# Kernel tuning notes

Hardware: AMD Instinct MI355X
Metric: run time of the kernel (lower is better)

The kernel has to match this reference:

```python
import jax, jax.numpy as jnp
import numpy as np

B, H, NI, NQ = 4096, 1024, 4096, 2048


def setup_inputs() -> dict:
    key = jax.random.key(0)
    ks = jax.random.split(key, 12)
    state = jax.random.normal(ks[0], (B, H), jnp.float32)
    inputX = jax.random.normal(ks[1], (B, NI), jnp.float32)
    # one-hot next-question vector
    q_idx = jax.random.randint(ks[2], (B,), 0, NQ)
    inputY = jax.nn.one_hot(q_idx, NQ, dtype=jnp.float32)
    truth = jax.random.bernoulli(ks[3], 0.5, (B,)).astype(jnp.float32)
    # torch.nn.Linear default init: U(-1/sqrt(fan_in), 1/sqrt(fan_in)), weight (out,in)
    def lin(kw, kb, out_d, in_d):
        bound = 1.0 / np.sqrt(in_d)
        W = jax.random.uniform(kw, (out_d, in_d), jnp.float32, -bound, bound)
        b = jax.random.uniform(kb, (out_d,), jnp.float32, -bound, bound)
        return W, b
    W_t, b_t = lin(ks[4], ks[5], H, H)    # transfer: n_hidden -> n_hidden
    W_x, b_x = lin(ks[6], ks[7], H, NI)   # linear_x: n_input -> n_hidden
    W_y, b_y = lin(ks[8], ks[9], NQ, H)   # linear_y: n_hidden -> n_questions
    return {"state": state, "inputX": inputX, "inputY": inputY, "truth": truth,
            "W_t": W_t, "b_t": b_t, "W_x": W_x, "b_x": b_x, "W_y": W_y, "b_y": b_y}


def reference(state, inputX, inputY, truth, W_t, b_t, W_x, b_x, W_y, b_y):
    # two small linears + tanh -> new hidden state
    linM = state @ W_t.T + b_t                       # (B, H)
    linX = inputX @ W_x.T + b_x                      # (B, H)
    hidden = jnp.tanh(linM + linX)                   # (B, H)
    # prediction head: linear + sigmoid, mask-select via one-hot sum
    pred_output = jax.nn.sigmoid(hidden @ W_y.T + b_y)  # (B, NQ)
    pred = jnp.sum(pred_output * inputY, axis=1)        # (B,)
    # binary cross entropy, sum reduction; torch clamps log terms at -100
    log_p = jnp.maximum(jnp.log(pred), -100.0)
    log_1mp = jnp.maximum(jnp.log1p(-pred), -100.0)
    err = -jnp.sum(truth * log_p + (1.0 - truth) * log_1mp)
    return (pred, err, hidden)
```

## Files before the change

kernel.cpp:

```cpp
#include <hip/hip_runtime.h>
#include <stdint.h>
#include <math.h>

#define B_DIM 4096
#define H_DIM 1024
#define NI_DIM 4096
#define NQ_DIM 2048
#define K_DIM 5120
#define NKT 160

typedef __attribute__((ext_vector_type(8))) short short8;
typedef __attribute__((ext_vector_type(4))) float f32x4;

__device__ __forceinline__ unsigned short f2bf(float f) {
  unsigned u = __float_as_uint(f);
  u += 0x7FFFu + ((u >> 16) & 1u);
  return (unsigned short)(u >> 16);
}
__device__ __forceinline__ float bf2f(unsigned short s) {
  return __uint_as_float(((unsigned)s) << 16);
}
__device__ __forceinline__ unsigned pkbf(float a, float b) {
  unsigned r;
  asm("v_cvt_pk_bf16_f32 %0, %1, %2" : "=v"(r) : "v"(a), "v"(b));
  return r;
}

__device__ __forceinline__ void gload_lds16(const void* g, void* l) {
  __builtin_amdgcn_global_load_lds(
      (__attribute__((address_space(1))) void*)(uintptr_t)g,
      (__attribute__((address_space(3))) void*)l, 16, 0, 0);
}

__global__ __launch_bounds__(256) void cast_v4(
    const float* __restrict__ X0, const float* __restrict__ X1,
    const float* __restrict__ W0, const float* __restrict__ W1,
    short* __restrict__ Xc, short* __restrict__ Wc) {
  __shared__ __align__(16) short lds[16384];
  int bt = blockIdx.x;
  const float *s0, *s1;
  short* dst;
  if (bt < (B_DIM / 128) * (NKT / 4)) { s0 = X0; s1 = X1; dst = Xc; }
  else { bt -= (B_DIM / 128) * (NKT / 4); s0 = W0; s1 = W1; dst = Wc; }
  const int rowTile = bt / (NKT / 4);
  const int K0 = (bt % (NKT / 4)) * 4;
  const float* src;
  int cols, colBase;
  if (K0 < 32) { src = s0; cols = 1024; colBase = K0 * 32; }
  else         { src = s1; cols = 4096; colBase = (K0 - 32) * 32; }
  const int tid = threadIdx.x;
  const int kc = tid & 31;
  const int r0 = tid >> 5;
#pragma unroll
  for (int i = 0; i < 16; ++i) {
    int r = r0 + i * 8;
    float4 v = *(const float4*)(src +
        (long long)(rowTile * 128 + r) * cols + colBase + kc * 4);
    uint2 o;
    o.x = pkbf(v.x, v.y);
    o.y = pkbf(v.z, v.w);
    int l = (kc >> 1) * 128 + r;
    int p = l ^ ((l >> 7) & 7);
    *(uint2*)(&lds[p * 8 + (kc & 1) * 4]) = o;
  }
  __syncthreads();
  short* dbase = dst + ((long long)rowTile * NKT + K0) * 4096;
#pragma unroll
  for (int i = 0; i < 8; ++i) {
    int c = tid + i * 256;
    int p = c ^ ((c >> 7) & 7);
    *(short8*)(dbase + c * 8) = *(const short8*)(&lds[p * 8]);
  }
}

__device__ __forceinline__ int ep_swz(int col, int rw) {
  int byte = col * 512 + rw * 2;
  byte ^= ((col ^ (col >> 3)) & 7) << 4;
  return byte;
}

__global__ __launch_bounds__(512, 2) void gemm_256(
    const short* __restrict__ Xc, const short* __restrict__ Wc,
    short* __restrict__ P, int ntile) {
  __shared__ __align__(16) short SH[65536];
  const int tid = threadIdx.x;
  const int lane = tid & 63;
  const int wid = tid >> 6;
  const int wr = wid >> 2, wc = wid & 3;
  const int fr = lane & 15, fq = lane >> 4;

  const int nwg = gridDim.x;
  const int orig = blockIdx.x;
  const int cpx = nwg >> 3;
  const int swz = (orig & 7) * cpx + (orig >> 3);
  const int bz = swz >> 6;
  const int bm = (swz >> 2) & 15;
  const int bn = swz & 3;
  const int kt0 = bz * (2 * ntile);

  const short* gA0 = Xc + ((long long)((bm * 2 + 0) * NKT + kt0) << 12);
  const short* gA2 = Xc + ((long long)((bm * 2 + 1) * NKT + kt0) << 12);
  const short* gB0 = Wc + ((long long)((bn * 2 + 0) * NKT + kt0) << 12);
  const short* gB2 = Wc + ((long long)((bn * 2 + 1) * NKT + kt0) << 12);

  f32x4 acc[8][4] = {};

  const int t8 = tid * 8;

  {
    gload_lds16(gA0 + t8, &SH[t8]);
    gload_lds16(gA0 + 4096 + t8, &SH[4096 + t8]);
    gload_lds16(gA2 + t8, &SH[8192 + t8]);
    gload_lds16(gA2 + 4096 + t8, &SH[12288 + t8]);
    gload_lds16(gB0 + t8, &SH[16384 + t8]);
    gload_lds16(gB0 + 4096 + t8, &SH[20480 + t8]);
    gload_lds16(gB2 + t8, &SH[24576 + t8]);
    gload_lds16(gB2 + 4096 + t8, &SH[28672 + t8]);
  }
  __syncthreads();

  int cur = 0;
  for (int t = 0; t < ntile; ++t) {
    if (t + 1 < ntile) {
      long long off = (long long)(t + 1) * 8192 + t8;
      short* L = &SH[(cur ^ 1) * 32768];
      gload_lds16(gA0 + off, L + t8);
      gload_lds16(gA0 + 4096 + off, L + 4096 + t8);
      gload_lds16(gA2 + off, L + 8192 + t8);
      gload_lds16(gA2 + 4096 + off, L + 12288 + t8);
      gload_lds16(gB0 + off, L + 16384 + t8);
      gload_lds16(gB0 + 4096 + off, L + 20480 + t8);
      gload_lds16(gB2 + off, L + 24576 + t8);
      gload_lds16(gB2 + 4096 + off, L + 28672 + t8);
    }
    const short* aS = &SH[cur * 32768] + wr * 8192;
    const short* bS = &SH[cur * 32768 + 16384] + (wc >> 1) * 8192;
    const int brow = (wc & 1) * 64;
#pragma unroll
    for (int ks = 0; ks < 2; ++ks) {
      short8 av[8], bv[4];
#pragma unroll
      for (int mi = 0; mi < 8; ++mi)
        av[mi] = *(const short8*)(aS + ks * 4096 +
                                  (fq * 128 + mi * 16 + fr) * 8);
#pragma unroll
      for (int ni = 0; ni < 4; ++ni)
        bv[ni] = *(const short8*)(bS + ks * 4096 +
                                  (fq * 128 + brow + ni * 16 + fr) * 8);
#pragma unroll
      for (int mi = 0; mi < 8; ++mi)
#pragma unroll
        for (int ni = 0; ni < 4; ++ni)
          acc[mi][ni] = __builtin_amdgcn_mfma_f32_16x16x32_bf16(
              av[mi], bv[ni], acc[mi][ni], 0, 0, 0);
    }
    __syncthreads();
    cur ^= 1;
  }

#pragma unroll
  for (int ni = 0; ni < 4; ++ni) {
    int col = wc * 64 + ni * 16 + fr;
#pragma unroll
    for (int mi = 0; mi < 8; ++mi) {
      int rw = wr * 128 + mi * 16 + fq * 4;
      uint2 pk;
      pk.x = (unsigned)f2bf(acc[mi][ni][0]) |
             ((unsigned)f2bf(acc[mi][ni][1]) << 16);
      pk.y = (unsigned)f2bf(acc[mi][ni][2]) |
             ((unsigned)f2bf(acc[mi][ni][3]) << 16);
      *(uint2*)((char*)SH + ep_swz(col, rw)) = pk;
    }
  }
  __syncthreads();
  short* Pp = P + (long long)bz * B_DIM * H_DIM;
#pragma unroll
  for (int h = 0; h < 16; ++h) {
    int chunk = tid + h * 512;
    int rr = chunk >> 5;
    int j = chunk & 31;
    short8 o;
#pragma unroll
    for (int k = 0; k < 8; ++k) {
      o[k] = *(const short*)((char*)SH + ep_swz(j * 8 + k, rr));
    }
    *(short8*)(Pp + (long long)(bm * 256 + rr) * H_DIM + bn * 256 + j * 8) = o;
  }
}

__global__ __launch_bounds__(256) void fuse_row(
    const short* __restrict__ P, const float* __restrict__ bt,
    const float* __restrict__ bx, const float* __restrict__ Y,
    const float* __restrict__ truth, const float* __restrict__ Wy,
    const float* __restrict__ by, float* __restrict__ predOut,
    float* __restrict__ hidden, float* __restrict__ bce, int S) {
  const int b = blockIdx.x;
  const int tid = threadIdx.x;
  __shared__ int s_cnt;
  __shared__ int s_idx[8];
  __shared__ float s_val[8];
  __shared__ float s_red[4];
  if (tid == 0) s_cnt = 0;

  const int c = tid * 4;
  float s0 = 0.f, s1 = 0.f, s2 = 0.f, s3 = 0.f;
  for (int z = 0; z < S; ++z) {
    const short* Pr = P + ((long long)z * B_DIM + b) * H_DIM + c;
    uint2 u = *(const uint2*)Pr;
    s0 += bf2f((unsigned short)(u.x & 0xffff));
    s1 += bf2f((unsigned short)(u.x >> 16));
    s2 += bf2f((unsigned short)(u.y & 0xffff));
    s3 += bf2f((unsigned short)(u.y >> 16));
  }
  float4 bt4 = *(const float4*)(bt + c);
  float4 bx4 = *(const float4*)(bx + c);
  float h0 = tanhf(s0 + bt4.x + bx4.x);
  float h1 = tanhf(s1 + bt4.y + bx4.y);
  float h2 = tanhf(s2 + bt4.z + bx4.z);
  float h3 = tanhf(s3 + bt4.w + bx4.w);
  float* Hr = hidden + (long long)b * H_DIM + c;
  Hr[0] = h0; Hr[1] = h1; Hr[2] = h2; Hr[3] = h3;

  __syncthreads();
  const float4* Yr = (const float4*)(Y + (long long)b * NQ_DIM);
#pragma unroll
  for (int hh = 0; hh < NQ_DIM / 4 / 256; ++hh) {
    int j = tid + hh * 256;
    float4 v = Yr[j];
    if (v.x != 0.0f) { int p = atomicAdd(&s_cnt, 1); if (p < 8) { s_idx[p] = 4 * j;     s_val[p] = v.x; } }
    if (v.y != 0.0f) { int p = atomicAdd(&s_cnt, 1); if (p < 8) { s_idx[p] = 4 * j + 1; s_val[p] = v.y; } }
    if (v.z != 0.0f) { int p = atomicAdd(&s_cnt, 1); if (p < 8) { s_idx[p] = 4 * j + 2; s_val[p] = v.z; } }
    if (v.w != 0.0f) { int p = atomicAdd(&s_cnt, 1); if (p < 8) { s_idx[p] = 4 * j + 3; s_val[p] = v.w; } }
  }
  __syncthreads();
  int cnt = s_cnt < 8 ? s_cnt : 8;
  float predv = 0.0f;
  for (int it = 0; it < cnt; ++it) {
    int q = s_idx[it];
    float4 w = *(const float4*)(Wy + (long long)q * H_DIM + c);
    float part = h0 * w.x + h1 * w.y + h2 * w.z + h3 * w.w;
#pragma unroll
    for (int off = 32; off > 0; off >>= 1) part += __shfl_down(part, off, 64);
    if ((tid & 63) == 0) s_red[tid >> 6] = part;
    __syncthreads();
    if (tid == 0) {
      float z = s_red[0] + s_red[1] + s_red[2] + s_red[3] + by[q];
      float p = 1.0f / (1.0f + expf(-z));
      predv += s_val[it] * p;
    }
    __syncthreads();
  }
  if (tid == 0) {
    predOut[b] = predv;
    float t = truth[b];
    float lp = fmaxf(logf(predv), -100.0f);
    float l1p = fmaxf(log1pf(-predv), -100.0f);
    bce[b] = -(t * lp + (1.0f - t) * l1p);
  }
}

__global__ __launch_bounds__(256) void reduce_err(
    const float* __restrict__ bce, float* __restrict__ errOut) {
  float s = 0.0f;
  for (int i = threadIdx.x; i < B_DIM; i += 256) s += bce[i];
#pragma unroll
  for (int off = 32; off > 0; off >>= 1) s += __shfl_down(s, off, 64);
  __shared__ float red[4];
  if ((threadIdx.x & 63) == 0) red[threadIdx.x >> 6] = s;
  __syncthreads();
  if (threadIdx.x == 0) errOut[0] = red[0] + red[1] + red[2] + red[3];
}

extern "C" void kernel_launch(void* const* d_in, const int* in_sizes, int n_in,
                              void* d_out, int out_size, void* d_ws, size_t ws_size,
                              hipStream_t stream) {
  (void)in_sizes; (void)n_in; (void)out_size;
  const float* state  = (const float*)d_in[0];
  const float* inputX = (const float*)d_in[1];
  const float* inputY = (const float*)d_in[2];
  const float* truth  = (const float*)d_in[3];
  const float* W_t    = (const float*)d_in[4];
  const float* b_t    = (const float*)d_in[5];
  const float* W_x    = (const float*)d_in[6];
  const float* b_x    = (const float*)d_in[7];
  const float* W_y    = (const float*)d_in[8];
  const float* b_y    = (const float*)d_in[9];

  const size_t XC_B = (size_t)B_DIM * K_DIM * 2;
  const size_t WC_B = (size_t)H_DIM * K_DIM * 2;
  const size_t PART = (size_t)B_DIM * H_DIM * 2;

  int S = 1;
  if (ws_size >= XC_B + WC_B + 4 * PART + 16384) S = 4;
  else if (ws_size >= XC_B + WC_B + 2 * PART + 16384) S = 2;

  short* Xc = (short*)d_ws;
  short* Wc = (short*)((char*)d_ws + XC_B);
  short* P  = (short*)((char*)d_ws + XC_B + WC_B);
  float* bce = (float*)((char*)d_ws + XC_B + WC_B + (size_t)S * PART);

  float* predOut = (float*)d_out;
  float* errOut  = predOut + B_DIM;
  float* hidden  = predOut + B_DIM + 1;

  cast_v4<<<(B_DIM / 128 + H_DIM / 128) * (NKT / 4), 256, 0, stream>>>(
      state, inputX, W_t, W_x, Xc, Wc);

  gemm_256<<<64 * S, 512, 0, stream>>>(Xc, Wc, P, 80 / S);

  fuse_row<<<B_DIM, 256, 0, stream>>>(P, b_t, b_x, inputY, truth, W_y, b_y,
                                      predOut, hidden, bce, S);
  reduce_err<<<1, 256, 0, stream>>>(bce, errOut);
}
```

Before: 92.51 us.

## Replace double-buffered GEMM loop with 4-slot async load pipeline

The bf16 GEMM main loop moves from a two-buffer scheme with 64-wide K steps to a four-slot ring of 32-wide K tiles, prefetching three tiles ahead. It uses explicit vmcnt waits and raw s_barrier in place of __syncthreads, and raises wave priority around the MFMA block with s_setprio. The goal is to hide global-to-LDS load latency better and keep MFMA issue dense. In exchange it runs twice as many iterations and barriers per K range, and correctness depends on the hand-counted vmcnt values matching the four loads issued per stage.

```diff
diff --git a/kernel.cpp b/kernel.cpp
--- a/kernel.cpp
+++ b/kernel.cpp
@@ -79,9 +79,9 @@
   return byte;
 }
 
-__global__ __launch_bounds__(512, 2) void gemm_256(
+__global__ __launch_bounds__(512, 2) void gemm_256p(
     const short* __restrict__ Xc, const short* __restrict__ Wc,
-    short* __restrict__ P, int ntile) {
+    short* __restrict__ P, int NT) {
   __shared__ __align__(16) short SH[65536];
   const int tid = threadIdx.x;
   const int lane = tid & 63;
@@ -96,67 +96,63 @@
   const int bz = swz >> 6;
   const int bm = (swz >> 2) & 15;
   const int bn = swz & 3;
-  const int kt0 = bz * (2 * ntile);
+  const int kt0 = bz * NT;
 
   const short* gA0 = Xc + ((long long)((bm * 2 + 0) * NKT + kt0) << 12);
-  const short* gA2 = Xc + ((long long)((bm * 2 + 1) * NKT + kt0) << 12);
+  const short* gA1 = Xc + ((long long)((bm * 2 + 1) * NKT + kt0) << 12);
   const short* gB0 = Wc + ((long long)((bn * 2 + 0) * NKT + kt0) << 12);
-  const short* gB2 = Wc + ((long long)((bn * 2 + 1) * NKT + kt0) << 12);
+  const short* gB1 = Wc + ((long long)((bn * 2 + 1) * NKT + kt0) << 12);
+
+  const int t8 = tid * 8;
+
+#define STAGE(tt)                                                        \
+  {                                                                      \
+    long long o = ((long long)(tt) << 12) + t8;                          \
+    short* L = &SH[((tt) & 3) * 16384];                                  \
+    gload_lds16(gA0 + o, L + t8);                                        \
+    gload_lds16(gA1 + o, L + 4096 + t8);                                 \
+    gload_lds16(gB0 + o, L + 8192 + t8);                                 \
+    gload_lds16(gB1 + o, L + 12288 + t8);                                \
+  }
 
   f32x4 acc[8][4] = {};
 
-  const int t8 = tid * 8;
-
-  {
-    gload_lds16(gA0 + t8, &SH[t8]);
-    gload_lds16(gA0 + 4096 + t8, &SH[4096 + t8]);
-    gload_lds16(gA2 + t8, &SH[8192 + t8]);
-    gload_lds16(gA2 + 4096 + t8, &SH[12288 + t8]);
-    gload_lds16(gB0 + t8, &SH[16384 + t8]);
-    gload_lds16(gB0 + 4096 + t8, &SH[20480 + t8]);
-    gload_lds16(gB2 + t8, &SH[24576 + t8]);
-    gload_lds16(gB2 + 4096 + t8, &SH[28672 + t8]);
-  }
-  __syncthreads();
-
-  int cur = 0;
-  for (int t = 0; t < ntile; ++t) {
-    if (t + 1 < ntile) {
-      long long off = (long long)(t + 1) * 8192 + t8;
-      short* L = &SH[(cur ^ 1) * 32768];
-      gload_lds16(gA0 + off, L + t8);
-      gload_lds16(gA0 + 4096 + off, L + 4096 + t8);
-      gload_lds16(gA2 + off, L + 8192 + t8);
-      gload_lds16(gA2 + 4096 + off, L + 12288 + t8);
-      gload_lds16(gB0 + off, L + 16384 + t8);
-      gload_lds16(gB0 + 4096 + off, L + 20480 + t8);
-      gload_lds16(gB2 + off, L + 24576 + t8);
-      gload_lds16(gB2 + 4096 + off, L + 28672 + t8);
-    }
-    const short* aS = &SH[cur * 32768] + wr * 8192;
-    const short* bS = &SH[cur * 32768 + 16384] + (wc >> 1) * 8192;
+  STAGE(0);
+  if (NT > 1) STAGE(1);
+  if (NT > 2) STAGE(2);
+
+  for (int t = 0; t < NT; ++t) {
+    if (t + 3 < NT) STAGE(t + 3);
+    int rem = NT - 1 - t;
+    if (rem >= 3)      asm volatile("s_waitcnt vmcnt(12)" ::: "memory");
+    else if (rem == 2) asm volatile("s_waitcnt vmcnt(8)" ::: "memory");
+    else if (rem == 1) asm volatile("s_waitcnt vmcnt(4)" ::: "memory");
+    else               asm volatile("s_waitcnt vmcnt(0)" ::: "memory");
+    __builtin_amdgcn_s_barrier();
+
+    const short* slot = &SH[(t & 3) * 16384];
+    const short* aS = slot + wr * 4096;
+    const short* bS = slot + 8192 + (wc >> 1) * 4096;
     const int brow = (wc & 1) * 64;
-#pragma unroll
-    for (int ks = 0; ks < 2; ++ks) {
-      short8 av[8], bv[4];
-#pragma unroll
-      for (int mi = 0; mi < 8; ++mi)
-        av[mi] = *(const short8*)(aS + ks * 4096 +
-                                  (fq * 128 + mi * 16 + fr) * 8);
+    short8 av[8], bv[4];
+#pragma unroll
+    for (int mi = 0; mi < 8; ++mi)
+      av[mi] = *(const short8*)(aS + (fq * 128 + mi * 16 + fr) * 8);
+#pragma unroll
+    for (int ni = 0; ni < 4; ++ni)
+      bv[ni] = *(const short8*)(bS + (fq * 128 + brow + ni * 16 + fr) * 8);
+
+    __builtin_amdgcn_s_setprio(1);
+#pragma unroll
+    for (int mi = 0; mi < 8; ++mi)
 #pragma unroll
       for (int ni = 0; ni < 4; ++ni)
-        bv[ni] = *(const short8*)(bS + ks * 4096 +
-                                  (fq * 128 + brow + ni * 16 + fr) * 8);
-#pragma unroll
-      for (int mi = 0; mi < 8; ++mi)
-#pragma unroll
-        for (int ni = 0; ni < 4; ++ni)
-          acc[mi][ni] = __builtin_amdgcn_mfma_f32_16x16x32_bf16(
-              av[mi], bv[ni], acc[mi][ni], 0, 0, 0);
-    }
-    __syncthreads();
-    cur ^= 1;
-  }
+        acc[mi][ni] = __builtin_amdgcn_mfma_f32_16x16x32_bf16(
+            av[mi], bv[ni], acc[mi][ni], 0, 0, 0);
+    __builtin_amdgcn_s_setprio(0);
+    __builtin_amdgcn_s_barrier();
+  }
+#undef STAGE
 
 #pragma unroll
   for (int ni = 0; ni < 4; ++ni) {
@@ -306,7 +302,7 @@
   cast_v4<<<(B_DIM / 128 + H_DIM / 128) * (NKT / 4), 256, 0, stream>>>(
       state, inputX, W_t, W_x, Xc, Wc);
 
-  gemm_256<<<64 * S, 512, 0, stream>>>(Xc, Wc, P, 80 / S);
+  gemm_256p<<<64 * S, 512, 0, stream>>>(Xc, Wc, P, NKT / S);
 
   fuse_row<<<B_DIM, 256, 0, stream>>>(P, b_t, b_x, inputY, truth, W_y, b_y,
                                       predOut, hidden, bce, S);
```

Measured after the change: 96.51 us. 1.04x slower.
